# Optimization experiments

Hardware: AMD Instinct MI355X
Metric: run time of the kernel (lower is better)

The kernel has to match this reference:

```python
import jax, jax.numpy as jnp
import numpy as np
from jax import lax


def setup_inputs() -> dict:
    key = jax.random.key(0)
    k1, k2, k3 = jax.random.split(key, 3)
    tens = jax.random.normal(k1, (16, 16, 128, 128), dtype=jnp.float32)
    filters = jax.random.normal(k2, (8, 1, 5, 5), dtype=jnp.float32)
    shifts = jax.random.randint(k3, (8, 2), 0, 5)  # (row_shift, col_shift) per group
    return {"tens": tens, "filters": filters, "shifts": shifts, "shift": 0, "filter_block": 0}


def _shifted_conv(tens, filters, shifts):
    B, C, H, W = tens.shape
    S = shifts.shape[0]
    kh, kw = filters.shape[-2], filters.shape[-1]
    # collapse batch and channel: each input channel treated independently
    x = tens.reshape(B * C, H, W)
    # pad right by kw-1, bottom by kh-1 (matches ConstantPad2d([0, kw-1, 0, kh-1]))
    xp = jnp.pad(x, ((0, 0), (0, kh - 1), (0, kw - 1)))
    Hp, Wp = H + kh - 1, W + kw - 1
    # non-cyclic roll: out[s, y, x] = xp[y - sy, x - sx], zero out-of-range
    ry = jnp.arange(Hp)[None, :] - shifts[:, 0][:, None]  # [S, Hp]
    rx = jnp.arange(Wp)[None, :] - shifts[:, 1][:, None]  # [S, Wp]
    vy = (ry >= 0) & (ry < Hp)
    vx = (rx >= 0) & (rx < Wp)
    ryc = jnp.clip(ry, 0, Hp - 1)
    rxc = jnp.clip(rx, 0, Wp - 1)
    # gather-shift: [N, S, Hp, Wp]
    shifted = xp[:, ryc[:, :, None], rxc[:, None, :]]
    mask = (vy[:, :, None] & vx[:, None, :])[None]  # [1, S, Hp, Wp]
    shifted = jnp.where(mask, shifted, jnp.zeros((), shifted.dtype))
    # grouped conv, one filter per shift group; VALID conv restores HxW
    out = lax.conv_general_dilated(
        shifted, filters, window_strides=(1, 1), padding='VALID',
        dimension_numbers=('NCHW', 'OIHW', 'NCHW'), feature_group_count=S)
    return out.reshape(B, C * S, H, W)


def reference(tens, filters, shifts, shift, filter_block):
    # `shift` and `filter_block` are unused by the original forward
    return _shifted_conv(tens, filters, shifts)
```

## Files before the change

### kernel.cpp

```cpp
#include <hip/hip_runtime.h>

#define H 128
#define W 128
#define NS 8
#define TR 8
#define LR 16
#define LC 136


__global__ __launch_bounds__(256) void shifted_conv_v2(
    const float* __restrict__ tens,
    const float* __restrict__ filters,
    const int*   __restrict__ shifts,
    float* __restrict__ out)
{
    __shared__ float lds[LR][LC];

    int blk  = blockIdx.x;
    int tile = blk & 15;
    int bc   = blk >> 4;
    int i0   = tile * TR;

    int tid = threadIdx.x;

    {
        int r      = tid >> 4;
        int c4base = tid & 15;
        int y = i0 - 4 + r;
        const float4* grow = (const float4*)(tens + (size_t)bc * (H * W) + y * W);
        bool yok = (unsigned)y < (unsigned)H;
        #pragma unroll
        for (int rep = 0; rep < 3; ++rep) {
            int c4 = c4base + rep * 16;
            if (c4 < 34) {
                float4 v = make_float4(0.f, 0.f, 0.f, 0.f);
                int x4 = c4 - 1;
                if (yok && (unsigned)x4 < 32u) v = grow[x4];
                *(float4*)&lds[r][c4 * 4] = v;
            }
        }
    }
    __syncthreads();

    int it = tid >> 5;
    int jt = tid & 31;
    int j0 = jt * 4;

    float* obase = out + (size_t)bc * (NS * H * W) + (size_t)(i0 + it) * W + j0;

    #pragma unroll
    for (int s = 0; s < NS; ++s) {
        int sy = shifts[2 * s];
        int sx = shifts[2 * s + 1];

        float acc0 = 0.f, acc1 = 0.f, acc2 = 0.f, acc3 = 0.f;

        #pragma unroll
        for (int u = 0; u < 5; ++u) {
            float g[9];
            #pragma unroll
            for (int m = 0; m < 9; ++m) {
                int v = m - 4 + sx;
                g[m] = ((unsigned)v < 5u) ? filters[s * 25 + u * 5 + v] : 0.f;
            }

            int row = it + u + 4 - sy;
            const float* rp = &lds[row][j0];
            float4 w0 = *(const float4*)(rp);
            float4 w1 = *(const float4*)(rp + 4);
            float4 w2 = *(const float4*)(rp + 8);
            float wb[12] = {w0.x, w0.y, w0.z, w0.w,
                            w1.x, w1.y, w1.z, w1.w,
                            w2.x, w2.y, w2.z, w2.w};

            #pragma unroll
            for (int m = 0; m < 9; ++m) {
                float fv = g[m];
                acc0 = fmaf(fv, wb[m + 0], acc0);
                acc1 = fmaf(fv, wb[m + 1], acc1);
                acc2 = fmaf(fv, wb[m + 2], acc2);
                acc3 = fmaf(fv, wb[m + 3], acc3);
            }
        }

        *(float4*)(obase + (size_t)s * (H * W)) = make_float4(acc0, acc1, acc2, acc3);
    }
}

extern "C" void kernel_launch(void* const* d_in, const int* in_sizes, int n_in,
                              void* d_out, int out_size, void* d_ws, size_t ws_size,
                              hipStream_t stream) {
    const float* tens    = (const float*)d_in[0];
    const float* filters = (const float*)d_in[1];
    const int*   shifts  = (const int*)d_in[2];
    float* out = (float*)d_out;

    shifted_conv_v2<<<256 * 16, 256, 0, stream>>>(tens, filters, shifts, out);
}
```

Before: 213.0 us.

## Precompute shifted filter taps and reuse each LDS row across all shift groups

A small pre-kernel builds a zero-padded table of shifted filter taps for each (row offset, group, column) into a device global. The main kernel then loops over the 9 possible row offsets, loading each LDS row window once and applying it to all 8 shift groups. A warp-uniform readfirstlane check skips row offsets that do not apply to a group. This cuts redundant LDS reads and the per-thread bounds logic on filter indexing. In exchange it adds a second launch and raises register pressure with 32 live accumulators.

```diff
diff --git a/kernel.cpp b/kernel.cpp
--- a/kernel.cpp
+++ b/kernel.cpp
@@ -7,10 +7,29 @@
 #define LR 16
 #define LC 136
 
+__device__ float g_gt[9 * 8 * 16];
 
-__global__ __launch_bounds__(256) void shifted_conv_v2(
+__global__ __launch_bounds__(256) void build_gt(
+    const float* __restrict__ filters,
+    const int*   __restrict__ shifts)
+{
+    int t = blockIdx.x * 256 + threadIdx.x;
+    if (t >= 9 * 8 * 16) return;
+    int m  = t & 15;
+    int s  = (t >> 4) & 7;
+    int dy = t >> 7;
+    float val = 0.f;
+    if (m < 9) {
+        int u = dy - 4 + shifts[2 * s];
+        int v = m - 4 + shifts[2 * s + 1];
+        if ((unsigned)u < 5u && (unsigned)v < 5u)
+            val = filters[s * 25 + u * 5 + v];
+    }
+    g_gt[t] = val;
+}
+
+__global__ __launch_bounds__(256) void shifted_conv_v3(
     const float* __restrict__ tens,
-    const float* __restrict__ filters,
     const int*   __restrict__ shifts,
     float* __restrict__ out)
 {
@@ -40,51 +59,55 @@
             }
         }
     }
+
+    int sy[NS];
+    #pragma unroll
+    for (int s = 0; s < NS; ++s)
+        sy[s] = __builtin_amdgcn_readfirstlane(shifts[2 * s]);
+
     __syncthreads();
 
     int it = tid >> 5;
     int jt = tid & 31;
     int j0 = jt * 4;
 
-    float* obase = out + (size_t)bc * (NS * H * W) + (size_t)(i0 + it) * W + j0;
+    float acc[NS][4];
+    #pragma unroll
+    for (int s = 0; s < NS; ++s)
+        #pragma unroll
+        for (int k = 0; k < 4; ++k) acc[s][k] = 0.f;
+
+    const float* rp = &lds[it][j0];
 
     #pragma unroll
-    for (int s = 0; s < NS; ++s) {
-        int sy = shifts[2 * s];
-        int sx = shifts[2 * s + 1];
-
-        float acc0 = 0.f, acc1 = 0.f, acc2 = 0.f, acc3 = 0.f;
+    for (int dy = 0; dy < 9; ++dy) {
+        float4 w0 = *(const float4*)(rp + dy * LC);
+        float4 w1 = *(const float4*)(rp + dy * LC + 4);
+        float4 w2 = *(const float4*)(rp + dy * LC + 8);
+        float w[12] = {w0.x, w0.y, w0.z, w0.w,
+                       w1.x, w1.y, w1.z, w1.w,
+                       w2.x, w2.y, w2.z, w2.w};
 
         #pragma unroll
-        for (int u = 0; u < 5; ++u) {
-            float g[9];
-            #pragma unroll
-            for (int m = 0; m < 9; ++m) {
-                int v = m - 4 + sx;
-                g[m] = ((unsigned)v < 5u) ? filters[s * 25 + u * 5 + v] : 0.f;
-            }
-
-            int row = it + u + 4 - sy;
-            const float* rp = &lds[row][j0];
-            float4 w0 = *(const float4*)(rp);
-            float4 w1 = *(const float4*)(rp + 4);
-            float4 w2 = *(const float4*)(rp + 8);
-            float wb[12] = {w0.x, w0.y, w0.z, w0.w,
-                            w1.x, w1.y, w1.z, w1.w,
-                            w2.x, w2.y, w2.z, w2.w};
-
-            #pragma unroll
-            for (int m = 0; m < 9; ++m) {
-                float fv = g[m];
-                acc0 = fmaf(fv, wb[m + 0], acc0);
-                acc1 = fmaf(fv, wb[m + 1], acc1);
-                acc2 = fmaf(fv, wb[m + 2], acc2);
-                acc3 = fmaf(fv, wb[m + 3], acc3);
+        for (int s = 0; s < NS; ++s) {
+            if ((unsigned)(dy - 4 + sy[s]) < 5u) {
+                #pragma unroll
+                for (int m = 0; m < 9; ++m) {
+                    float fv = g_gt[(dy * 8 + s) * 16 + m];
+                    acc[s][0] = fmaf(fv, w[m + 0], acc[s][0]);
+                    acc[s][1] = fmaf(fv, w[m + 1], acc[s][1]);
+                    acc[s][2] = fmaf(fv, w[m + 2], acc[s][2]);
+                    acc[s][3] = fmaf(fv, w[m + 3], acc[s][3]);
+                }
             }
         }
+    }
 
-        *(float4*)(obase + (size_t)s * (H * W)) = make_float4(acc0, acc1, acc2, acc3);
-    }
+    float* obase = out + (size_t)bc * (NS * H * W) + (size_t)(i0 + it) * W + j0;
+    #pragma unroll
+    for (int s = 0; s < NS; ++s)
+        *(float4*)(obase + (size_t)s * (H * W)) =
+            make_float4(acc[s][0], acc[s][1], acc[s][2], acc[s][3]);
 }
 
 extern "C" void kernel_launch(void* const* d_in, const int* in_sizes, int n_in,
@@ -95,5 +118,6 @@
     const int*   shifts  = (const int*)d_in[2];
     float* out = (float*)d_out;
 
-    shifted_conv_v2<<<256 * 16, 256, 0, stream>>>(tens, filters, shifts, out);
+    build_gt<<<(9 * 8 * 16 + 255) / 256, 256, 0, stream>>>(filters, shifts);
+    shifted_conv_v3<<<256 * 16, 256, 0, stream>>>(tens, shifts, out);
 }
```

Measured after the change: 178.2 us. 1.2x faster.
